# Kernel tuning notes

Measured on AMD Instinct MI355X. Metric: run time of the kernel, lower is better.

## Reference

```python
import jax, jax.numpy as jnp
import numpy as np

B, S, E, H = 2, 2048, 1024, 16
D = E // H  # head_dim = 64
ROPE_BASE = 10000.0


def _rope_tables(seq_len, head_dim, dtype):
    inv_freq = 1.0 / (ROPE_BASE ** (jnp.arange(0, head_dim, 2, dtype=jnp.float32) / head_dim))
    freqs = jnp.arange(seq_len, dtype=jnp.float32)[:, None] * inv_freq[None, :]  # [S, D/2]
    emb = jnp.concatenate([freqs, freqs], axis=-1)  # [S, D]
    return jnp.cos(emb).astype(dtype), jnp.sin(emb).astype(dtype)


def _rotate_half(x):
    x1, x2 = jnp.split(x, 2, axis=-1)
    return jnp.concatenate([-x2, x1], axis=-1)


def _apply_rope(x, cos, sin):
    # x: [B, H, S, D]; cos/sin: [S, D] broadcast over batch/heads
    return x * cos[None, None] + _rotate_half(x) * sin[None, None]


def setup_inputs() -> dict:
    key = jax.random.key(0)
    ks = jax.random.split(key, 10)
    sigma = 0.02
    return {
        "x": jax.random.normal(ks[0], (B, S, E), dtype=jnp.float32),
        "attn_mask": jnp.ones((B, S), dtype=jnp.int32),
        "Wq": jax.random.normal(ks[1], (E, E), dtype=jnp.float32) * sigma,
        "bq": jnp.zeros((E,), dtype=jnp.float32),
        "Wk": jax.random.normal(ks[2], (E, E), dtype=jnp.float32) * sigma,
        "bk": jnp.zeros((E,), dtype=jnp.float32),
        "Wv": jax.random.normal(ks[3], (E, E), dtype=jnp.float32) * sigma,
        "bv": jnp.zeros((E,), dtype=jnp.float32),
        "Wo": jax.random.normal(ks[4], (E, E), dtype=jnp.float32) * sigma,
        "bo": jnp.zeros((E,), dtype=jnp.float32),
    }


def reference(x, attn_mask, Wq, bq, Wk, bk, Wv, bv, Wo, bo):
    b, s, e = x.shape
    h, d = H, D

    def proj(W, bias):
        y = jnp.einsum("bse,ef->bsf", x, W) + bias
        return y.reshape(b, s, h, d).transpose(0, 2, 1, 3)  # [B,H,S,D]

    q = proj(Wq, bq)
    k = proj(Wk, bk)
    cos, sin = _rope_tables(s, d, x.dtype)
    q = _apply_rope(q, cos, sin)
    k = _apply_rope(k, cos, sin)
    v = proj(Wv, bv)

    scores = jnp.einsum("bhqd,bhkd->bhqk", q, k)
    # causal mask
    causal = jnp.triu(jnp.ones((s, s), dtype=bool), k=1)
    scores = jnp.where(causal[None, None], -jnp.inf, scores)
    # padding mask: attn_mask [B,S] -> [B,1,1,S], mask where 0
    pad = (attn_mask == 0)[:, None, None, :]
    scores = jnp.where(pad, -jnp.inf, scores)
    # NOTE: source divides by sqrt(k.shape[-1]) = sqrt(head_dim)
    attn_weights = jax.nn.softmax(scores / np.sqrt(d), axis=-1)
    out = jnp.einsum("bhqk,bhkd->bhqd", attn_weights, v)
    out = out.transpose(0, 2, 1, 3).reshape(b, s, e)
    return jnp.einsum("bse,ef->bsf", out, Wo) + bo
```

## Files before the change

kernel.cpp:

```cpp
#include <hip/hip_runtime.h>
#include <cmath>

#define B_ 2
#define S_ 2048
#define E_ 1024
#define H_ 16
#define D_ 64

typedef __attribute__((ext_vector_type(8)))  short  bf16x8;
typedef __attribute__((ext_vector_type(4)))  float  f32x4;
typedef __attribute__((ext_vector_type(16))) float  f32x16;
typedef __attribute__((ext_vector_type(8)))  unsigned short ushort8;
typedef __attribute__((ext_vector_type(4)))  unsigned short ushort4v;
typedef __attribute__((ext_vector_type(4)))  unsigned int   u32x4;
typedef unsigned int u32;

__device__ __forceinline__ ushort f2bf(float f) {
    u32 u = __float_as_uint(f);
    u32 r = (u + 0x7fffu + ((u >> 16) & 1u)) >> 16;
    return (ushort)r;
}
__device__ __forceinline__ void gload_lds16(const ushort* gp, ushort* lp) {
    auto g = (const __attribute__((address_space(1))) u32*)gp;
    auto l = (__attribute__((address_space(3))) u32*)lp;
    __builtin_amdgcn_global_load_lds(g, l, 16, 0, 0);
}
__device__ __forceinline__ u32 cvtpk_bf16(float lo, float hi) {
    u32 r;
    asm("v_cvt_pk_bf16_f32 %0, %1, %2" : "=v"(r) : "v"(lo), "v"(hi));
    return r;
}
__device__ __forceinline__ float hw_exp2(float x) {
    float r;
    asm("v_exp_f32 %0, %1" : "=v"(r) : "v"(x));
    return r;
}
__device__ __forceinline__ void hw_sincos_rev(float rev, float* sn, float* cs) {
    float fr;
    asm("v_fract_f32 %0, %1" : "=v"(fr) : "v"(rev));
    asm("v_sin_f32 %0, %1" : "=v"(*sn) : "v"(fr));
    asm("v_cos_f32 %0, %1" : "=v"(*cs) : "v"(fr));
}

__global__ __launch_bounds__(256) void fused_casts(
    const float* __restrict__ x, ushort* __restrict__ xb,
    const float* __restrict__ Wq, const float* __restrict__ Wk,
    const float* __restrict__ Wv, const float* __restrict__ Wo,
    ushort* __restrict__ WtQKV, ushort* __restrict__ WtO)
{
    __shared__ float tile[64][33];

    if (blockIdx.x < 2048) {
        const int idx = blockIdx.x * 256 + threadIdx.x;
        const float4 a = *reinterpret_cast<const float4*>(&x[(size_t)idx * 8]);
        const float4 b = *reinterpret_cast<const float4*>(&x[(size_t)idx * 8 + 4]);
        ushort8 o;
        o[0] = f2bf(a.x); o[1] = f2bf(a.y); o[2] = f2bf(a.z); o[3] = f2bf(a.w);
        o[4] = f2bf(b.x); o[5] = f2bf(b.y); o[6] = f2bf(b.z); o[7] = f2bf(b.w);
        *reinterpret_cast<ushort8*>(&xb[(size_t)idx * 8]) = o;
        return;
    }

    const int lin = blockIdx.x - 2048;
    const int z   = lin >> 9;
    const int rem = lin & 511;
    const int by  = rem >> 5;
    const int bx  = rem & 31;

    const float* src; ushort* dst;
    switch (z) {
        case 0:  src = Wq; dst = WtQKV;                 break;
        case 1:  src = Wk; dst = WtQKV + 1024 * 1024;   break;
        case 2:  src = Wv; dst = WtQKV + 2048 * 1024;   break;
        default: src = Wo; dst = WtO;                   break;
    }
    const int k0 = by * 64, n0 = bx * 32;
    const int tn = threadIdx.x & 31, tk = threadIdx.x >> 5;
    #pragma unroll
    for (int p = 0; p < 8; ++p)
        tile[p * 8 + tk][tn] = src[(size_t)(k0 + p * 8 + tk) * 1024 + n0 + tn];
    __syncthreads();
    const int kp = (threadIdx.x & 31) * 2, nq = threadIdx.x >> 5;
    #pragma unroll
    for (int q = 0; q < 4; ++q) {
        const int n = q * 8 + nq;
        const u32 v = (u32)f2bf(tile[kp][n]) | ((u32)f2bf(tile[kp + 1][n]) << 16);
        *reinterpret_cast<u32*>(&dst[(size_t)(n0 + n) * 1024 + k0 + kp]) = v;
    }
}

__global__ __launch_bounds__(256, 3) void gemm_qkv(
    const ushort* __restrict__ A, const ushort* __restrict__ Bt,
    const float* __restrict__ bq, const float* __restrict__ bk,
    const float* __restrict__ bv,
    ushort* __restrict__ Qb, ushort* __restrict__ Kb, ushort* __restrict__ Vt)
{
    __shared__ ushort As[128 * 64];
    __shared__ ushort Bs[128 * 64];
    const int t = threadIdx.x, w = t >> 6, l = t & 63;
    const int lr = l & 15, lg = l >> 4;
    const int wr = w >> 1, wc = w & 1;

    const int lin  = blockIdx.y * 24 + blockIdx.x;
    const int xcd  = lin & 7;
    const int slot = lin >> 3;
    const int row0 = (xcd * 4 + slot / 24) * 128;
    const int col0 = (slot % 24) * 128;

    f32x4 acc[4][4] = {};

    for (int k0 = 0; k0 < 1024; k0 += 64) {
        #pragma unroll
        for (int i = 0; i < 4; ++i) {
            const int r  = w * 32 + i * 8 + (l >> 3);
            const int cs = ((l & 7) ^ (r & 7)) * 8;
            gload_lds16(&A [(size_t)(row0 + r) * 1024 + k0 + cs], &As[(w * 32 + i * 8) * 64]);
            gload_lds16(&Bt[(size_t)(col0 + r) * 1024 + k0 + cs], &Bs[(w * 32 + i * 8) * 64]);
        }
        asm volatile("s_waitcnt vmcnt(0)");
        __syncthreads();

        #pragma unroll
        for (int kk = 0; kk < 2; ++kk) {
            bf16x8 af[4], bfr[4];
            #pragma unroll
            for (int m = 0; m < 4; ++m)
                af[m] = *reinterpret_cast<const bf16x8*>(
                    &As[(wr * 64 + m * 16 + lr) * 64 + (((kk * 4 + lg) ^ (lr & 7)) * 8)]);
            #pragma unroll
            for (int n = 0; n < 4; ++n)
                bfr[n] = *reinterpret_cast<const bf16x8*>(
                    &Bs[(wc * 64 + n * 16 + lr) * 64 + (((kk * 4 + lg) ^ (lr & 7)) * 8)]);
            #pragma unroll
            for (int m = 0; m < 4; ++m)
                #pragma unroll
                for (int n = 0; n < 4; ++n)
                    acc[m][n] = __builtin_amdgcn_mfma_f32_16x16x32_bf16(
                        af[m], bfr[n], acc[m][n], 0, 0, 0);
        }
        __syncthreads();
    }

    const int cbase = col0 + wc * 64;
    const int cls   = cbase >> 10;
    const int hcol  = cbase & 1023;
    const float* bias = (cls == 0) ? bq : (cls == 1 ? bk : bv);

    if (cls < 2) {
        ushort* dst = (cls == 0) ? Qb : Kb;
        const float qscale = (cls == 0) ? 0.1803368801f : 1.0f;
        #pragma unroll
        for (int m = 0; m < 4; ++m) {
            const int rbase = row0 + wr * 64 + m * 16 + lg * 4;
            #pragma unroll
            for (int n = 0; n < 2; ++n) {
                const int i    = n * 16 + lr;
                const float b0 = bias[hcol + i];
                const float b1 = bias[hcol + i + 32];
                const float invf_rev =
                    exp2f(-(float)i * 0.415241012f) * 0.15915494309f;
                #pragma unroll
                for (int r = 0; r < 4; ++r) {
                    const int row = rbase + r;
                    const int s   = row & (S_ - 1);
                    float sn, cs_;
                    hw_sincos_rev((float)s * invf_rev, &sn, &cs_);
                    const float v0 = acc[m][n][r]     + b0;
                    const float v1 = acc[m][n + 2][r] + b1;
                    dst[(size_t)row * 1024 + hcol + i]      = f2bf((v0 * cs_ - v1 * sn) * qscale);
                    dst[(size_t)row * 1024 + hcol + i + 32] = f2bf((v1 * cs_ + v0 * sn) * qscale);
                }
            }
        }
    } else {
        const int h = hcol >> 6;
        #pragma unroll
        for (int m = 0; m < 4; ++m) {
            const int rbase = row0 + wr * 64 + m * 16 + lg * 4;
            const int bb = rbase >> 11, s0 = rbase & (S_ - 1);
            #pragma unroll
            for (int n = 0; n < 4; ++n) {
                const int d = n * 16 + lr;
                const float bia = bias[hcol + d];
                ushort4v pk;
                #pragma unroll
                for (int r = 0; r < 4; ++r) pk[r] = f2bf(acc[m][n][r] + bia);
                *reinterpret_cast<ushort4v*>(
                    &Vt[((size_t)(bb * 16 + h) * 64 + d) * S_ + s0]) = pk;
            }
        }
    }
}

__global__ __launch_bounds__(256, 1) void gemm_out(
    const ushort* __restrict__ A, const ushort* __restrict__ Bt,
    const float* __restrict__ bias, float* __restrict__ C, int N, int K)
{
    __shared__ ushort As[2][128 * 64];
    __shared__ ushort Bs[2][128 * 64];
    const int t = threadIdx.x, w = t >> 6, l = t & 63;
    const int lr = l & 15, lg = l >> 4;
    const int wr = w >> 1, wc = w & 1;
    const int row0 = blockIdx.y * 128, col0 = blockIdx.x * 128;

    f32x4 acc[4][4] = {};

    auto STAGE = [&](int buf, int k0) {
        #pragma unroll
        for (int i = 0; i < 4; ++i) {
            const int r  = w * 32 + i * 8 + (l >> 3);
            const int cs = ((l & 7) ^ (r & 7)) * 8;
            gload_lds16(&A [(size_t)(row0 + r) * K + k0 + cs], &As[buf][(w * 32 + i * 8) * 64]);
            gload_lds16(&Bt[(size_t)(col0 + r) * K + k0 + cs], &Bs[buf][(w * 32 + i * 8) * 64]);
        }
    };

    STAGE(0, 0);
    int cur = 0;

    for (int k0 = 0; k0 < K; k0 += 64) {
        if (k0 + 64 < K) {
            STAGE(cur ^ 1, k0 + 64);
            asm volatile("s_waitcnt vmcnt(8)" ::: "memory");
        } else {
            asm volatile("s_waitcnt vmcnt(0)" ::: "memory");
        }
        __builtin_amdgcn_s_barrier();

        #pragma unroll
        for (int kk = 0; kk < 2; ++kk) {
            bf16x8 af[4], bfr[4];
            #pragma unroll
            for (int m = 0; m < 4; ++m)
                af[m] = *reinterpret_cast<const bf16x8*>(
                    &As[cur][(wr * 64 + m * 16 + lr) * 64 + (((kk * 4 + lg) ^ (lr & 7)) * 8)]);
            #pragma unroll
            for (int n = 0; n < 4; ++n)
                bfr[n] = *reinterpret_cast<const bf16x8*>(
                    &Bs[cur][(wc * 64 + n * 16 + lr) * 64 + (((kk * 4 + lg) ^ (lr & 7)) * 8)]);
            #pragma unroll
            for (int m = 0; m < 4; ++m)
                #pragma unroll
                for (int n = 0; n < 4; ++n)
                    acc[m][n] = __builtin_amdgcn_mfma_f32_16x16x32_bf16(
                        af[m], bfr[n], acc[m][n], 0, 0, 0);
        }
        __builtin_amdgcn_s_barrier();
        cur ^= 1;
    }

    #pragma unroll
    for (int m = 0; m < 4; ++m) {
        const int rbase = row0 + wr * 64 + m * 16 + lg * 4;
        #pragma unroll
        for (int n = 0; n < 4; ++n) {
            const int c = col0 + wc * 64 + n * 16 + lr;
            const float bv = bias[c];
            #pragma unroll
            for (int r = 0; r < 4; ++r)
                C[(size_t)(rbase + r) * N + c] = acc[m][n][r] + bv;
        }
    }
}

__global__ __launch_bounds__(256, 2) void attn13(
    const ushort* __restrict__ Qb, const ushort* __restrict__ Kb,
    const ushort* __restrict__ Vt, ushort* __restrict__ AO)
{
    __shared__ ushort Ks[2][128 * 64];
    __shared__ ushort Vs[2][64 * 128];

    const int t = threadIdx.x, w = t >> 6, l = t & 63;
    const int lq = l & 31, hi = l >> 5;
    const int idx = blockIdx.x;
    const int bh = idx & 31, b = bh >> 4, h = bh & 15;
    const int g8 = idx >> 5;
    const int qb = (idx < 256) ? (15 - g8) : (g8 - 8);
    const int q0 = qb * 128, qw = q0 + w * 32;
    const int qg = qw + lq;

    const ushort* Kbh = Kb + (size_t)b * S_ * 1024 + h * 64;
    const ushort* Vbh = Vt + (size_t)bh * 64 * S_;

    bf16x8 qf[4];
    {
        const ushort* qrow = Qb + (size_t)(b * S_ + qg) * 1024 + h * 64 + 8 * hi;
        #pragma unroll
        for (int dc = 0; dc < 4; ++dc)
            qf[dc] = *reinterpret_cast<const bf16x8*>(qrow + 16 * dc);
    }

    f32x16 oacc[2] = {};
    float mrow = -3.0e38f, lrow = 0.f;

    auto STAGE = [&](int buf, int kt) {
        #pragma unroll
        for (int i = 0; i < 4; ++i) {
            const int cid = i * 256 + t;
            const int r   = cid >> 3;
            const int cs  = ((cid & 7) ^ (r & 7)) * 8;
            const int db  = (i * 256 + w * 64) * 8;
            gload_lds16(&Kbh[(size_t)(kt + r) * 1024 + cs], &Ks[buf][db]);
        }
        #pragma unroll
        for (int i = 0; i < 4; ++i) {
            const int cid = i * 256 + t;
            const int d   = cid >> 4;
            const int cs  = ((cid & 15) ^ (d & 15)) * 8;
            const int db  = (i * 256 + w * 64) * 8;
            gload_lds16(&Vbh[(size_t)d * S_ + kt + cs], &Vs[buf][db]);
        }
    };

    const int kend = q0 + 128;
    STAGE(0, 0);
    int cur = 0;

    for (int kt = 0; kt < kend; kt += 128) {
        if (kt + 128 < kend) {
            STAGE(cur ^ 1, kt + 128);
            asm volatile("s_waitcnt vmcnt(8)" ::: "memory");
        } else {
            asm volatile("s_waitcnt vmcnt(0)" ::: "memory");
        }
        __builtin_amdgcn_s_barrier();

        {
            const ushort* Kc = &Ks[cur][0];
            const ushort* Vc = &Vs[cur][0];

            f32x16 sacc[4] = {};
            __builtin_amdgcn_s_setprio(1);
            #pragma unroll
            for (int sub = 0; sub < 4; ++sub) {
                const int rK = sub * 32 + lq;
                const int rx = lq & 7;
                #pragma unroll
                for (int dc = 0; dc < 4; ++dc) {
                    const bf16x8 kf = *reinterpret_cast<const bf16x8*>(
                        &Kc[rK * 64 + (((2 * dc + hi) ^ rx) * 8)]);
                    sacc[sub] = __builtin_amdgcn_mfma_f32_32x32x16_bf16(
                        kf, qf[dc], sacc[sub], 0, 0, 0);
                }
            }
            __builtin_amdgcn_s_setprio(0);

            #pragma unroll
            for (int hf = 0; hf < 2; ++hf) {
                const int sA = 2 * hf, sB = 2 * hf + 1;

                #pragma unroll
                for (int sub = sA; sub <= sB; ++sub)
                    if (kt + sub * 32 + 31 > qw) {
                        #pragma unroll
                        for (int r = 0; r < 16; ++r) {
                            const int kg = kt + sub * 32 + (r & 3) + 8 * (r >> 2) + 4 * hi;
                            if (kg > qg) sacc[sub][r] = -1.0e30f;
                        }
                    }

                float mx[16];
                #pragma unroll
                for (int r = 0; r < 16; ++r)
                    mx[r] = fmaxf(sacc[sA][r], sacc[sB][r]);
                #pragma unroll
                for (int s2 = 8; s2 > 0; s2 >>= 1)
                    #pragma unroll
                    for (int r = 0; r < s2; ++r) mx[r] = fmaxf(mx[r], mx[r + s2]);
                const float tm = fmaxf(mx[0], __shfl_xor(mx[0], 32));

                if (!__all(tm <= mrow)) {
                    const float mnew = fmaxf(mrow, tm);
                    const float corr = hw_exp2(mrow - mnew);
                    lrow *= corr;
                    #pragma unroll
                    for (int r = 0; r < 16; ++r) { oacc[0][r] *= corr; oacc[1][r] *= corr; }
                    mrow = mnew;
                }

                float sm[16];
                #pragma unroll
                for (int sub = sA; sub <= sB; ++sub)
                    #pragma unroll
                    for (int r = 0; r < 16; ++r)
                        sacc[sub][r] = hw_exp2(sacc[sub][r] - mrow);
                #pragma unroll
                for (int r = 0; r < 16; ++r) sm[r] = sacc[sA][r] + sacc[sB][r];
                #pragma unroll
                for (int s2 = 8; s2 > 0; s2 >>= 1)
                    #pragma unroll
                    for (int r = 0; r < s2; ++r) sm[r] += sm[r + s2];
                lrow += sm[0] + __shfl_xor(sm[0], 32);

                #pragma unroll
                for (int sub = sA; sub <= sB; ++sub) {
                    u32 wpk[8];
                    #pragma unroll
                    for (int i = 0; i < 8; ++i)
                        wpk[i] = cvtpk_bf16(sacc[sub][2 * i], sacc[sub][2 * i + 1]);
                    u32 a0 = wpk[0], b0 = wpk[2];
                    u32 a1 = wpk[1], b1 = wpk[3];
                    u32 a2 = wpk[4], b2 = wpk[6];
                    u32 a3 = wpk[5], b3 = wpk[7];
                    asm("v_permlane32_swap_b32 %0, %1" : "+v"(a0), "+v"(b0));
                    asm("v_permlane32_swap_b32 %0, %1" : "+v"(a1), "+v"(b1));
                    asm("v_permlane32_swap_b32 %0, %1" : "+v"(a2), "+v"(b2));
                    asm("v_permlane32_swap_b32 %0, %1" : "+v"(a3), "+v"(b3));
                    u32x4 pw0, pw1;
                    pw0[0] = a0; pw0[1] = a1; pw0[2] = b0; pw0[3] = b1;
                    pw1[0] = a2; pw1[1] = a3; pw1[2] = b2; pw1[3] = b3;
                    const bf16x8 pb0 = __builtin_bit_cast(bf16x8, pw0);
                    const bf16x8 pb1 = __builtin_bit_cast(bf16x8, pw1);
                    __builtin_amdgcn_s_setprio(1);
                    #pragma unroll
                    for (int dt = 0; dt < 2; ++dt) {
                        const int rV = dt * 32 + lq;
                        const int jx = lq & 15;
                        const bf16x8 v0 = *reinterpret_cast<const bf16x8*>(
                            &Vc[rV * 128 + (((sub * 4 + 0 * 2 + hi) ^ jx) * 8)]);
                        oacc[dt] = __builtin_amdgcn_mfma_f32_32x32x16_bf16(
                            v0, pb0, oacc[dt], 0, 0, 0);
                        const bf16x8 v1 = *reinterpret_cast<const bf16x8*>(
                            &Vc[rV * 128 + (((sub * 4 + 1 * 2 + hi) ^ jx) * 8)]);
                        oacc[dt] = __builtin_amdgcn_mfma_f32_32x32x16_bf16(
                            v1, pb1, oacc[dt], 0, 0, 0);
                    }
                    __builtin_amdgcn_s_setprio(0);
                }
            }
        }
        __builtin_amdgcn_s_barrier();
        cur ^= 1;
    }

    const float inv = 1.f / lrow;
    ushort* aorow = AO + (size_t)(b * S_ + qg) * 1024 + h * 64;
    #pragma unroll
    for (int dt = 0; dt < 2; ++dt)
        #pragma unroll
        for (int g = 0; g < 4; ++g) {
            const int d0 = dt * 32 + g * 8 + hi * 4;
            ushort4v pk;
            #pragma unroll
            for (int j = 0; j < 4; ++j) pk[j] = f2bf(oacc[dt][g * 4 + j] * inv);
            *reinterpret_cast<ushort4v*>(&aorow[d0]) = pk;
        }
}

extern "C" void kernel_launch(void* const* d_in, const int* in_sizes, int n_in,
                              void* d_out, int out_size, void* d_ws, size_t ws_size,
                              hipStream_t stream)
{
    const float* x  = (const float*)d_in[0];
    const float* Wq = (const float*)d_in[2];
    const float* bq = (const float*)d_in[3];
    const float* Wk = (const float*)d_in[4];
    const float* bk = (const float*)d_in[5];
    const float* Wv = (const float*)d_in[6];
    const float* bv = (const float*)d_in[7];
    const float* Wo = (const float*)d_in[8];
    const float* bo = (const float*)d_in[9];
    float* out = (float*)d_out;

    const size_t tok = (size_t)B_ * S_;
    ushort* xb    = (ushort*)d_ws;
    ushort* WtQKV = xb + tok * E_;
    ushort* WtO   = WtQKV + (size_t)3072 * 1024;
    ushort* Qb    = WtO + (size_t)1024 * 1024;
    ushort* Kb    = Qb + tok * E_;
    ushort* Vt    = Kb + tok * E_;
    ushort* AO    = Vt + tok * E_;

    fused_casts<<<4096, 256, 0, stream>>>(x, xb, Wq, Wk, Wv, Wo, WtQKV, WtO);

    gemm_qkv<<<dim3(24, 32), 256, 0, stream>>>(xb, WtQKV, bq, bk, bv, Qb, Kb, Vt);

    attn13<<<512, 256, 0, stream>>>(Qb, Kb, Vt, AO);

    gemm_out<<<dim3(8, 32), 256, 0, stream>>>(AO, WtO, bo, out, 1024, 1024);
}
```

Before: 105.5 us.

## Split long causal query tiles across two blocks and merge partial softmax outputs

The attention kernel grows from 512 to 768 blocks. Query tiles 0-7 run whole, and tiles 8-15 have their KV tiles split into even and odd halves processed by separate blocks. Each split block writes an unnormalized bf16 partial output plus its running max and sum, and a new merge kernel combines the two halves into the attention output. The KV buffer drops from double to single buffering so three blocks can fit per CU. This is meant to balance work under the causal mask, at the cost of losing copy/compute overlap within a block, an extra launch, bf16 rounding of the partial outputs, and reuse of workspace buffers that gemm_qkv is already done with.

```diff
diff --git a/kernel.cpp b/kernel.cpp
--- a/kernel.cpp
+++ b/kernel.cpp
@@ -19,6 +19,9 @@
     u32 u = __float_as_uint(f);
     u32 r = (u + 0x7fffu + ((u >> 16) & 1u)) >> 16;
     return (ushort)r;
+}
+__device__ __forceinline__ float bf2f(ushort u) {
+    return __uint_as_float(((u32)u) << 16);
 }
 __device__ __forceinline__ void gload_lds16(const ushort* gp, ushort* lp) {
     auto g = (const __attribute__((address_space(1))) u32*)gp;
@@ -263,21 +266,27 @@
     }
 }
 
-__global__ __launch_bounds__(256, 2) void attn13(
+__global__ __launch_bounds__(256, 3) void attn14(
     const ushort* __restrict__ Qb, const ushort* __restrict__ Kb,
-    const ushort* __restrict__ Vt, ushort* __restrict__ AO)
+    const ushort* __restrict__ Vt, ushort* __restrict__ AO,
+    ushort* __restrict__ PartO, float2* __restrict__ PartML)
 {
-    __shared__ ushort Ks[2][128 * 64];
-    __shared__ ushort Vs[2][64 * 128];
+    __shared__ ushort Ks[128 * 64];
+    __shared__ ushort Vs[64 * 128];
 
     const int t = threadIdx.x, w = t >> 6, l = t & 63;
     const int lq = l & 31, hi = l >> 5;
     const int idx = blockIdx.x;
-    const int bh = idx & 31, b = bh >> 4, h = bh & 15;
-    const int g8 = idx >> 5;
-    const int qb = (idx < 256) ? (15 - g8) : (g8 - 8);
+    const int g = idx >> 8;
+    const int j = idx & 255;
+    const int bh = j & 31, b = bh >> 4, h = bh & 15;
+    const int qq = j >> 5;
+    const int qb     = (g == 0) ? qq : (15 - qq);
+    const int tstart = (g == 2) ? 1 : 0;
+    const int tstep  = (g == 0) ? 1 : 2;
     const int q0 = qb * 128, qw = q0 + w * 32;
     const int qg = qw + lq;
+    const int nt = qb + 1;
 
     const ushort* Kbh = Kb + (size_t)b * S_ * 1024 + h * 64;
     const ushort* Vbh = Vt + (size_t)bh * 64 * S_;
@@ -293,14 +302,14 @@
     f32x16 oacc[2] = {};
     float mrow = -3.0e38f, lrow = 0.f;
 
-    auto STAGE = [&](int buf, int kt) {
+    auto STAGE = [&](int kt) {
         #pragma unroll
         for (int i = 0; i < 4; ++i) {
             const int cid = i * 256 + t;
             const int r   = cid >> 3;
             const int cs  = ((cid & 7) ^ (r & 7)) * 8;
             const int db  = (i * 256 + w * 64) * 8;
-            gload_lds16(&Kbh[(size_t)(kt + r) * 1024 + cs], &Ks[buf][db]);
+            gload_lds16(&Kbh[(size_t)(kt + r) * 1024 + cs], &Ks[db]);
         }
         #pragma unroll
         for (int i = 0; i < 4; ++i) {
@@ -308,26 +317,19 @@
             const int d   = cid >> 4;
             const int cs  = ((cid & 15) ^ (d & 15)) * 8;
             const int db  = (i * 256 + w * 64) * 8;
-            gload_lds16(&Vbh[(size_t)d * S_ + kt + cs], &Vs[buf][db]);
+            gload_lds16(&Vbh[(size_t)d * S_ + kt + cs], &Vs[db]);
         }
     };
 
-    const int kend = q0 + 128;
-    STAGE(0, 0);
-    int cur = 0;
-
-    for (int kt = 0; kt < kend; kt += 128) {
-        if (kt + 128 < kend) {
-            STAGE(cur ^ 1, kt + 128);
-            asm volatile("s_waitcnt vmcnt(8)" ::: "memory");
-        } else {
-            asm volatile("s_waitcnt vmcnt(0)" ::: "memory");
-        }
+    for (int tt = tstart; tt < nt; tt += tstep) {
+        const int kt = tt * 128;
+        STAGE(kt);
+        asm volatile("s_waitcnt vmcnt(0)" ::: "memory");
         __builtin_amdgcn_s_barrier();
 
         {
-            const ushort* Kc = &Ks[cur][0];
-            const ushort* Vc = &Vs[cur][0];
+            const ushort* Kc = &Ks[0];
+            const ushort* Vc = &Vs[0];
 
             f32x16 sacc[4] = {};
             __builtin_amdgcn_s_setprio(1);
@@ -430,21 +432,65 @@
             }
         }
         __builtin_amdgcn_s_barrier();
-        cur ^= 1;
-    }
-
-    const float inv = 1.f / lrow;
-    ushort* aorow = AO + (size_t)(b * S_ + qg) * 1024 + h * 64;
+    }
+
+    if (g == 0) {
+        const float inv = 1.f / lrow;
+        ushort* aorow = AO + (size_t)(b * S_ + qg) * 1024 + h * 64;
+        #pragma unroll
+        for (int dt = 0; dt < 2; ++dt)
+            #pragma unroll
+            for (int gg = 0; gg < 4; ++gg) {
+                const int d0 = dt * 32 + gg * 8 + hi * 4;
+                ushort4v pk;
+                #pragma unroll
+                for (int jj = 0; jj < 4; ++jj) pk[jj] = f2bf(oacc[dt][gg * 4 + jj] * inv);
+                *reinterpret_cast<ushort4v*>(&aorow[d0]) = pk;
+            }
+    } else {
+        const int s    = g - 1;
+        const int prow = (bh << 10) + (qg - 1024);
+        PartML[(size_t)s * 32768 + prow] = make_float2(mrow, lrow);
+        ushort* po = PartO + ((size_t)s * 32768 + prow) * 64;
+        #pragma unroll
+        for (int dt = 0; dt < 2; ++dt)
+            #pragma unroll
+            for (int gg = 0; gg < 4; ++gg) {
+                const int d0 = dt * 32 + gg * 8 + hi * 4;
+                ushort4v pk;
+                #pragma unroll
+                for (int jj = 0; jj < 4; ++jj) pk[jj] = f2bf(oacc[dt][gg * 4 + jj]);
+                *reinterpret_cast<ushort4v*>(&po[d0]) = pk;
+            }
+    }
+}
+
+__global__ __launch_bounds__(256) void merge_split(
+    const ushort* __restrict__ PartO, const float2* __restrict__ PartML,
+    ushort* __restrict__ AO)
+{
+    const int tid  = blockIdx.x * 256 + threadIdx.x;
+    const int prow = tid >> 4;
+    const int dq   = (tid & 15) * 4;
+
+    const float2 ml0 = PartML[prow];
+    const float2 ml1 = PartML[32768 + prow];
+    const float M  = fmaxf(ml0.x, ml1.x);
+    const float w0 = hw_exp2(ml0.x - M);
+    const float w1 = hw_exp2(ml1.x - M);
+    const float inv = 1.f / (ml0.y * w0 + ml1.y * w1);
+
+    const ushort4v o0 = *reinterpret_cast<const ushort4v*>(&PartO[(size_t)prow * 64 + dq]);
+    const ushort4v o1 = *reinterpret_cast<const ushort4v*>(&PartO[(size_t)(32768 + prow) * 64 + dq]);
+
+    const int bh = prow >> 10, qg = (prow & 1023) + 1024;
+    const int b = bh >> 4, h = bh & 15;
+    ushort4v outv;
     #pragma unroll
-    for (int dt = 0; dt < 2; ++dt)
-        #pragma unroll
-        for (int g = 0; g < 4; ++g) {
-            const int d0 = dt * 32 + g * 8 + hi * 4;
-            ushort4v pk;
-            #pragma unroll
-            for (int j = 0; j < 4; ++j) pk[j] = f2bf(oacc[dt][g * 4 + j] * inv);
-            *reinterpret_cast<ushort4v*>(&aorow[d0]) = pk;
-        }
+    for (int jj = 0; jj < 4; ++jj)
+        outv[jj] = f2bf((bf2f(o0[jj]) * w0 + bf2f(o1[jj]) * w1) * inv);
+    *reinterpret_cast<ushort4v*>(
+        &AO[(size_t)(b * S_ + qg) * 1024 + h * 64 + dq]) = outv;
 }
 
 extern "C" void kernel_launch(void* const* d_in, const int* in_sizes, int n_in,
@@ -470,12 +516,16 @@
     ushort* Kb    = Qb + tok * E_;
     ushort* Vt    = Kb + tok * E_;
     ushort* AO    = Vt + tok * E_;
+    ushort* PartO  = xb;
+    float2* PartML = (float2*)WtQKV;
 
     fused_casts<<<4096, 256, 0, stream>>>(x, xb, Wq, Wk, Wv, Wo, WtQKV, WtO);
 
     gemm_qkv<<<dim3(24, 32), 256, 0, stream>>>(xb, WtQKV, bq, bk, bv, Qb, Kb, Vt);
 
-    attn13<<<512, 256, 0, stream>>>(Qb, Kb, Vt, AO);
+    attn14<<<768, 256, 0, stream>>>(Qb, Kb, Vt, AO, PartO, PartML);
+
+    merge_split<<<2048, 256, 0, stream>>>(PartO, PartML, AO);
 
     gemm_out<<<dim3(8, 32), 256, 0, stream>>>(AO, WtO, bo, out, 1024, 1024);
 }
```

Measured after the change: 103.2 us (median of 3 runs). 2.2% less time.
